# Optimization experiments

Measured on AMD Instinct MI355X. Metric: run time of the kernel, lower is better.

## Reference

```python
import jax, jax.numpy as jnp
import numpy as np

# Constants mirroring HomeostasisConfig defaults + STDP module constants
TARGET_RATE = 0.05
TRACE_DECAY = float(np.exp(-1.0 / 20.0))   # tau_plus = tau_minus = 20
ACT_DECAY   = 0.999                        # activity_decay / firing-rate EMA
BETA        = 0.9                          # LIF membrane leak
ETA_TH      = 0.001                        # threshold_adaptation_rate
MIN_W, MAX_W = -5.0, 5.0
MIN_TH, MAX_TH = 0.5, 2.0
LR          = 1.0                          # STDP learning_rate
TAG_THRESH  = 1e-3

B, T, IN, OUT = 128, 64, 2048, 2048


def setup_inputs() -> dict:
    key = jax.random.key(0)
    k1, k2 = jax.random.split(key, 2)
    # Bernoulli(0.1) rate-coded input spike trains (batch, time, in_features)
    x = (jax.random.uniform(k1, (B, T, IN)) < 0.1).astype(jnp.float32)
    W = jax.random.normal(k2, (OUT, IN), dtype=jnp.float32) * 0.1
    thresholds = jnp.ones((OUT,), dtype=jnp.float32)
    A_plus = jnp.asarray(0.01, dtype=jnp.float32)
    A_minus = jnp.asarray(0.012, dtype=jnp.float32)
    return {"x": x, "W": W, "thresholds": thresholds,
            "A_plus": A_plus, "A_minus": A_minus}


def _step(carry, x_t, A_plus, A_minus):
    v, Wc, th, pre_tr, post_tr, post_act, fr_ema, tags = carry
    # LIF membrane: leak + synaptic current, threshold, reset
    v = BETA * v + x_t @ Wc.T                      # (B, OUT)
    spk = (v >= th).astype(v.dtype)                # (B, OUT)
    v = v * (1.0 - spk)
    # trace / activity updates (batch-mean rates, as in update_traces)
    pre_rate = x_t.mean(axis=0)                    # (IN,)
    post_rate = spk.mean(axis=0)                   # (OUT,)
    pre_tr = TRACE_DECAY * pre_tr + pre_rate
    post_tr = TRACE_DECAY * post_tr + post_rate
    post_act = ACT_DECAY * post_act + (1.0 - ACT_DECAY) * post_rate
    # STDP: LTP/LTD outer products
    ltp = jnp.outer(post_rate, pre_tr) * jnp.abs(A_plus)
    ltd = jnp.outer(post_tr, pre_rate) * jnp.abs(A_minus)
    dw = ltp - ltd                                 # (OUT, IN)
    # metaplasticity factor
    meta = 1.0 / jnp.clip(post_act / TARGET_RATE, 0.5, 2.0)
    dw = dw * meta[:, None]
    # soft bounds
    w_range = MAX_W - MIN_W
    dw_b = jnp.where(dw > 0, dw * (MAX_W - Wc) / w_range,
                     dw * (Wc - MIN_W) / w_range)
    # synaptic tags
    tags = jnp.maximum(0.99 * tags, (jnp.abs(dw_b) > TAG_THRESH).astype(v.dtype))
    # apply STDP + clamp
    Wc = jnp.clip(Wc + LR * dw_b, MIN_W, MAX_W)
    # intrinsic plasticity: threshold homeostasis
    fr_ema = ACT_DECAY * fr_ema + (1.0 - ACT_DECAY) * post_rate
    th = jnp.clip(th * (1.0 + ETA_TH * (post_rate - TARGET_RATE)), MIN_TH, MAX_TH)
    return (v, Wc, th, pre_tr, post_tr, post_act, fr_ema, tags), spk


def reference(x, W, thresholds, A_plus, A_minus):
    b, t, n_in = x.shape
    n_out = W.shape[0]
    dt = x.dtype
    carry0 = (
        jnp.zeros((b, n_out), dt),                 # membrane potential
        W,                                         # weights
        thresholds,                                # per-neuron thresholds
        jnp.zeros((n_in,), dt),                    # pre trace
        jnp.zeros((n_out,), dt),                   # post trace
        jnp.full((n_out,), TARGET_RATE, dt),       # post activity EMA
        jnp.full((n_out,), TARGET_RATE, dt),       # firing-rate EMA
        jnp.zeros((n_out, n_in), dt),              # synaptic tags
    )
    step = lambda c, xt: _step(c, xt, A_plus, A_minus)
    _, spikes = jax.lax.scan(step, carry0, jnp.swapaxes(x, 0, 1))
    return jnp.swapaxes(spikes, 0, 1)              # (B, T, OUT)
```

## Files before the change

### kernel.cpp

```cpp
#include <hip/hip_runtime.h>
#include <cmath>

#define B_   128
#define T_   64
#define IN_  2048
#define OUT_ 2048
#define IDXSTRIDE 512

#define BETA_D   0.9
#define ACTDEC_D 0.999
#define ETA_TH_D 0.001
#define TARGET_D 0.05
#define MINW_D   (-5.0)
#define MAXW_D   (5.0)
#define MINTH_D  0.5
#define MAXTH_D  2.0

#define SWADR(i) (((unsigned)(i) << 6) | ((((unsigned)(i) ^ ((unsigned)(i) >> 2)) & 3u) << 4))
#define VL_OFF   131072
#define TH_OFF   139264
#define PTR_OFF  139328
#define PACT_OFF 139392
#define COA_OFF  139456
#define COB_OFF  139520
#define PART_OFF 139584
#define SMEM_BYTES 139840

__global__ __launch_bounds__(256) void k_rate(const float* __restrict__ x,
                                              double* __restrict__ pre_rate) {
    int t = blockIdx.x;
    int i = blockIdx.y * 256 + threadIdx.x;
    const float* xp = x + (size_t)t * IN_ + i;
    float s = 0.f;
    for (int b = 0; b < B_; ++b) s += xp[(size_t)b * T_ * IN_];
    pre_rate[(size_t)t * IN_ + i] = (double)s * (1.0 / 128.0);
}

__global__ __launch_bounds__(256) void k_scan(const double* __restrict__ pre_rate,
                                              double* __restrict__ pre_tr, double decay) {
    int i = blockIdx.x * 256 + threadIdx.x;
    double tr = 0.0;
    for (int t = 0; t < T_; ++t) {
        tr = decay * tr + pre_rate[(size_t)t * IN_ + i];
        pre_tr[(size_t)t * IN_ + i] = tr;
    }
}

__global__ __launch_bounds__(256) void k_build_idx(const float* __restrict__ x,
        unsigned* __restrict__ idx, int* __restrict__ cnt) {
    int row  = blockIdx.x * 4 + (threadIdx.x >> 6);
    int lane = threadIdx.x & 63;
    const float* xr = x + (size_t)row * IN_;
    unsigned* ip = idx + (size_t)row * IDXSTRIDE;
    int c = 0;
    for (int ch = 0; ch < IN_ / 64; ++ch) {
        int i = ch * 64 + lane;
        float vv = xr[i];
        unsigned long long m = __ballot(vv != 0.0f);
        if (vv != 0.0f) {
            int pos = c + __popcll(m & ((1ull << lane) - 1ull));
            if (pos < IDXSTRIDE) ip[pos] = SWADR(i);
        }
        c += __popcll(m);
    }
    if (lane == 0) cnt[row] = (c < IDXSTRIDE) ? c : IDXSTRIDE;
}

#define GAT(r, A0, A1) do { \
    const double2 w_ = *(const double2*)(smem + ((r) ^ cx)); \
    A0 += w_.x; A1 += w_.y; } while (0)

__global__ __launch_bounds__(512, 1) void k_main(
        const float* __restrict__ W, const float* __restrict__ thr,
        const float* __restrict__ Ap, const float* __restrict__ Am,
        const unsigned* __restrict__ idx, const int* __restrict__ cnt,
        const double* __restrict__ pre_rate, const double* __restrict__ pre_tr,
        float* __restrict__ out, double decay) {
    extern __shared__ char smem[];
    double* vL    = (double*)(smem + VL_OFF);
    double* thL   = (double*)(smem + TH_OFF);
    double* ptrL  = (double*)(smem + PTR_OFF);
    double* pactL = (double*)(smem + PACT_OFF);
    double* coaL  = (double*)(smem + COA_OFF);
    double* cobL  = (double*)(smem + COB_OFF);
    float*  part  = (float*)(smem + PART_OFF);

    const int tid = threadIdx.x;
    const int s   = blockIdx.x;

#pragma unroll
    for (int o = 0; o < 8; ++o) {
        const float* wr = W + (size_t)(s * 8 + o) * IN_;
        for (int i = tid; i < IN_; i += 512) {
            *(double*)(smem + ((SWADR(i) ^ ((unsigned)(o >> 1) << 4)) | ((unsigned)(o & 1) << 3)))
                = (double)wr[i];
        }
    }
    for (int e = tid; e < B_ * 8; e += 512) vL[e] = 0.0;
    if (tid < 8) {
        thL[tid]   = (double)thr[s * 8 + tid];
        ptrL[tid]  = 0.0;
        pactL[tid] = TARGET_D;
    }
    const double apv = fabs((double)Ap[0]);
    const double amv = fabs((double)Am[0]);
    __syncthreads();

    const int b  = tid >> 2;
    const int c2 = tid & 3;
    const unsigned cx = (unsigned)c2 << 4;

    for (int t = 0; t < T_; ++t) {
        int row = b * T_ + t;
        int n = cnt[row];
        const unsigned* ip = idx + (size_t)row * IDXSTRIDE;
        double a0 = 0.0, a1 = 0.0, b0 = 0.0, b1 = 0.0;
        int n8 = n & ~7;
        int j = 0;
        if (n8 > 0) {
            uint4 q0 = *(const uint4*)(ip);
            uint4 q1 = *(const uint4*)(ip + 4);
            for (;;) {
                uint4 qa = q0, qb = q1;
                int jn = j + 8;
                if (jn < n8) {
                    q0 = *(const uint4*)(ip + jn);
                    q1 = *(const uint4*)(ip + jn + 4);
                }
                GAT(qa.x, a0, a1); GAT(qa.y, b0, b1);
                GAT(qa.z, a0, a1); GAT(qa.w, b0, b1);
                GAT(qb.x, a0, a1); GAT(qb.y, b0, b1);
                GAT(qb.z, a0, a1); GAT(qb.w, b0, b1);
                j = jn;
                if (j >= n8) break;
            }
        }
        for (; j < n; ++j) { unsigned r = ip[j]; GAT(r, a0, a1); }
        a0 += b0; a1 += b1;

        double2 vv = *(double2*)&vL[b * 8 + c2 * 2];
        double v0 = BETA_D * vv.x + a0;
        double v1 = BETA_D * vv.y + a1;
        double t0 = thL[c2 * 2], t1 = thL[c2 * 2 + 1];
        float s0 = (v0 >= t0) ? 1.0f : 0.0f;
        float s1 = (v1 >= t1) ? 1.0f : 0.0f;
        *(float2*)(out + (size_t)row * OUT_ + s * 8 + c2 * 2) = make_float2(s0, s1);
        vv.x = (s0 != 0.0f) ? 0.0 : v0;
        vv.y = (s1 != 0.0f) ? 0.0 : v1;
        *(double2*)&vL[b * 8 + c2 * 2] = vv;

        float r0 = s0, r1 = s1;
        r0 += __shfl_xor(r0, 4);  r1 += __shfl_xor(r1, 4);
        r0 += __shfl_xor(r0, 8);  r1 += __shfl_xor(r1, 8);
        r0 += __shfl_xor(r0, 16); r1 += __shfl_xor(r1, 16);
        r0 += __shfl_xor(r0, 32); r1 += __shfl_xor(r1, 32);
        if ((tid & 63) < 4)
            *(float2*)&part[(tid >> 6) * 8 + c2 * 2] = make_float2(r0, r1);
        __syncthreads();

        if (tid < 8) {
            int c = tid;
            float cf = 0.f;
#pragma unroll
            for (int w8 = 0; w8 < 8; ++w8) cf += part[w8 * 8 + c];
            double prate = (double)cf * (1.0 / 128.0);
            double ptr2 = decay * ptrL[c] + prate;            ptrL[c] = ptr2;
            double pact = ACTDEC_D * pactL[c] + (1.0 - ACTDEC_D) * prate;  pactL[c] = pact;
            double r = pact / TARGET_D;
            r = r < 0.5 ? 0.5 : (r > 2.0 ? 2.0 : r);
            double meta = 1.0 / r;
            coaL[c] = apv * prate * meta;
            cobL[c] = amv * ptr2 * meta;
            double thv = thL[c] * (1.0 + ETA_TH_D * (prate - TARGET_D));
            thL[c] = thv < MINTH_D ? MINTH_D : (thv > MAXTH_D ? MAXTH_D : thv);
        }
        __syncthreads();

        if (t + 1 < T_) {
            double ca0 = coaL[c2 * 2], ca1 = coaL[c2 * 2 + 1];
            double cb0 = cobL[c2 * 2], cb1 = cobL[c2 * 2 + 1];
            const double* prt = pre_tr   + (size_t)t * IN_;
            const double* prr = pre_rate + (size_t)t * IN_;
#pragma unroll 4
            for (int k = 0; k < 16; ++k) {
                int i = k * 128 + b;
                double p = prt[i], q = prr[i];
                double2* wp = (double2*)(smem + (SWADR(i) ^ cx));
                double2 w2 = *wp;
                double dw0 = ca0 * p - cb0 * q;
                double dw1 = ca1 * p - cb1 * q;
                double dwb0 = dw0 > 0.0 ? (dw0 * (MAXW_D - w2.x)) / 10.0
                                        : (dw0 * (w2.x - MINW_D)) / 10.0;
                double dwb1 = dw1 > 0.0 ? (dw1 * (MAXW_D - w2.y)) / 10.0
                                        : (dw1 * (w2.y - MINW_D)) / 10.0;
                double nw0 = w2.x + dwb0;
                nw0 = nw0 < MINW_D ? MINW_D : (nw0 > MAXW_D ? MAXW_D : nw0);
                double nw1 = w2.y + dwb1;
                nw1 = nw1 < MINW_D ? MINW_D : (nw1 > MAXW_D ? MAXW_D : nw1);
                *wp = make_double2(nw0, nw1);
            }
        }
        __syncthreads();
    }
}

extern "C" void kernel_launch(void* const* d_in, const int* in_sizes, int n_in,
                              void* d_out, int out_size, void* d_ws, size_t ws_size,
                              hipStream_t stream) {
    const float* x   = (const float*)d_in[0];
    const float* W   = (const float*)d_in[1];
    const float* thr = (const float*)d_in[2];
    const float* Ap  = (const float*)d_in[3];
    const float* Am  = (const float*)d_in[4];
    float* out = (float*)d_out;
    char* ws = (char*)d_ws;

    double* pre_rate = (double*)(ws);
    double* pre_tr   = (double*)(ws + 1048576);
    unsigned* idx    = (unsigned*)(ws + 2097152);
    int* cnt         = (int*)(ws + 2097152 + 16777216);

    double decay = std::exp(-1.0 / 20.0);

    (void)hipFuncSetAttribute((const void*)k_main,
                              hipFuncAttributeMaxDynamicSharedMemorySize, SMEM_BYTES);

    k_rate<<<dim3(T_, IN_ / 256), 256, 0, stream>>>(x, pre_rate);
    k_scan<<<IN_ / 256, 256, 0, stream>>>(pre_rate, pre_tr, decay);
    k_build_idx<<<(B_ * T_) / 4, 256, 0, stream>>>(x, idx, cnt);
    k_main<<<256, 512, SMEM_BYTES, stream>>>(W, thr, Ap, Am, idx, cnt,
                                             pre_rate, pre_tr, out, decay);
}
```

Before: 879.3 us.

## Split gather across two threads per output pair and drop serial stats phase

Block size goes from 512 to 1024 threads. The index list is split into even and odd halves, so two threads gather each batch/output pair and combine their sums with a shuffle. The per-neuron statistics (traces, activity, thresholds) are now held redundantly in registers by every thread instead of being computed by 8 threads between two barriers, which removes one __syncthreads per step. Spike counts go through double-buffered shared atomics. The shared-memory swizzle is dropped, which may raise bank conflicts; more waves may help hide LDS gather latency.

```diff
diff --git a/kernel.cpp b/kernel.cpp
--- a/kernel.cpp
+++ b/kernel.cpp
@@ -6,6 +6,7 @@
 #define IN_  2048
 #define OUT_ 2048
 #define IDXSTRIDE 512
+#define HALFSTRIDE 256
 
 #define BETA_D   0.9
 #define ACTDEC_D 0.999
@@ -16,15 +17,8 @@
 #define MINTH_D  0.5
 #define MAXTH_D  2.0
 
-#define SWADR(i) (((unsigned)(i) << 6) | ((((unsigned)(i) ^ ((unsigned)(i) >> 2)) & 3u) << 4))
-#define VL_OFF   131072
-#define TH_OFF   139264
-#define PTR_OFF  139328
-#define PACT_OFF 139392
-#define COA_OFF  139456
-#define COB_OFF  139520
-#define PART_OFF 139584
-#define SMEM_BYTES 139840
+#define PART_OFF   131072
+#define SMEM_BYTES 131136
 
 __global__ __launch_bounds__(256) void k_rate(const float* __restrict__ x,
                                               double* __restrict__ pre_rate) {
@@ -52,69 +46,80 @@
     int lane = threadIdx.x & 63;
     const float* xr = x + (size_t)row * IN_;
     unsigned* ip = idx + (size_t)row * IDXSTRIDE;
-    int c = 0;
+    const unsigned long long EVEN = 0x5555555555555555ull;
+    unsigned long long below = (1ull << lane) - 1ull;
+    int ce = 0, co = 0;
     for (int ch = 0; ch < IN_ / 64; ++ch) {
         int i = ch * 64 + lane;
         float vv = xr[i];
         unsigned long long m = __ballot(vv != 0.0f);
+        unsigned long long me = m & EVEN, mo = m & ~EVEN;
         if (vv != 0.0f) {
-            int pos = c + __popcll(m & ((1ull << lane) - 1ull));
-            if (pos < IDXSTRIDE) ip[pos] = SWADR(i);
-        }
-        c += __popcll(m);
-    }
-    if (lane == 0) cnt[row] = (c < IDXSTRIDE) ? c : IDXSTRIDE;
+            if ((lane & 1) == 0) {
+                int pos = ce + __popcll(me & below);
+                if (pos < HALFSTRIDE) ip[pos] = (unsigned)i << 6;
+            } else {
+                int pos = co + __popcll(mo & below);
+                if (pos < HALFSTRIDE) ip[HALFSTRIDE + pos] = (unsigned)i << 6;
+            }
+        }
+        ce += __popcll(me);
+        co += __popcll(mo);
+    }
+    if (lane == 0) {
+        if (ce > HALFSTRIDE) ce = HALFSTRIDE;
+        if (co > HALFSTRIDE) co = HALFSTRIDE;
+        cnt[row] = ce | (co << 16);
+    }
 }
 
 #define GAT(r, A0, A1) do { \
     const double2 w_ = *(const double2*)(smem + ((r) ^ cx)); \
     A0 += w_.x; A1 += w_.y; } while (0)
 
-__global__ __launch_bounds__(512, 1) void k_main(
+__global__ __launch_bounds__(1024, 4) void k_main(
         const float* __restrict__ W, const float* __restrict__ thr,
         const float* __restrict__ Ap, const float* __restrict__ Am,
         const unsigned* __restrict__ idx, const int* __restrict__ cnt,
         const double* __restrict__ pre_rate, const double* __restrict__ pre_tr,
         float* __restrict__ out, double decay) {
     extern __shared__ char smem[];
-    double* vL    = (double*)(smem + VL_OFF);
-    double* thL   = (double*)(smem + TH_OFF);
-    double* ptrL  = (double*)(smem + PTR_OFF);
-    double* pactL = (double*)(smem + PACT_OFF);
-    double* coaL  = (double*)(smem + COA_OFF);
-    double* cobL  = (double*)(smem + COB_OFF);
-    float*  part  = (float*)(smem + PART_OFF);
-
-    const int tid = threadIdx.x;
-    const int s   = blockIdx.x;
+    float* part = (float*)(smem + PART_OFF);
+
+    const int tid  = threadIdx.x;
+    const int s    = blockIdx.x;
+    const int lane = tid & 63;
+    const int h    = tid & 1;
+    const int c2   = (tid >> 1) & 3;
+    const int b    = tid >> 3;
+    const unsigned cx = (unsigned)c2 << 4;
 
 #pragma unroll
     for (int o = 0; o < 8; ++o) {
         const float* wr = W + (size_t)(s * 8 + o) * IN_;
-        for (int i = tid; i < IN_; i += 512) {
-            *(double*)(smem + ((SWADR(i) ^ ((unsigned)(o >> 1) << 4)) | ((unsigned)(o & 1) << 3)))
-                = (double)wr[i];
-        }
-    }
-    for (int e = tid; e < B_ * 8; e += 512) vL[e] = 0.0;
-    if (tid < 8) {
-        thL[tid]   = (double)thr[s * 8 + tid];
-        ptrL[tid]  = 0.0;
-        pactL[tid] = TARGET_D;
-    }
+        for (int i = tid; i < IN_; i += 1024) {
+            *(double*)(smem + (((unsigned)i << 6) | ((unsigned)(o >> 1) << 4)
+                               | ((unsigned)(o & 1) << 3))) = (double)wr[i];
+        }
+    }
+    if (tid < 16) part[tid] = 0.0f;
+
+    double th0 = (double)thr[s * 8 + c2 * 2];
+    double th1 = (double)thr[s * 8 + c2 * 2 + 1];
+    double ptr0 = 0.0, ptr1 = 0.0;
+    double pact0 = TARGET_D, pact1 = TARGET_D;
+    double vr0 = 0.0, vr1 = 0.0;
     const double apv = fabs((double)Ap[0]);
     const double amv = fabs((double)Am[0]);
     __syncthreads();
 
-    const int b  = tid >> 2;
-    const int c2 = tid & 3;
-    const unsigned cx = (unsigned)c2 << 4;
-
     for (int t = 0; t < T_; ++t) {
+        const int pb = t & 1;
         int row = b * T_ + t;
-        int n = cnt[row];
-        const unsigned* ip = idx + (size_t)row * IDXSTRIDE;
-        double a0 = 0.0, a1 = 0.0, b0 = 0.0, b1 = 0.0;
+        int cc = cnt[row];
+        int n = h ? (cc >> 16) : (cc & 0xffff);
+        const unsigned* ip = idx + (size_t)row * IDXSTRIDE + h * HALFSTRIDE;
+        double a0 = 0.0, a1 = 0.0, e0 = 0.0, e1 = 0.0;
         int n8 = n & ~7;
         int j = 0;
         if (n8 > 0) {
@@ -127,65 +132,73 @@
                     q0 = *(const uint4*)(ip + jn);
                     q1 = *(const uint4*)(ip + jn + 4);
                 }
-                GAT(qa.x, a0, a1); GAT(qa.y, b0, b1);
-                GAT(qa.z, a0, a1); GAT(qa.w, b0, b1);
-                GAT(qb.x, a0, a1); GAT(qb.y, b0, b1);
-                GAT(qb.z, a0, a1); GAT(qb.w, b0, b1);
+                GAT(qa.x, a0, a1); GAT(qa.y, e0, e1);
+                GAT(qa.z, a0, a1); GAT(qa.w, e0, e1);
+                GAT(qb.x, a0, a1); GAT(qb.y, e0, e1);
+                GAT(qb.z, a0, a1); GAT(qb.w, e0, e1);
                 j = jn;
                 if (j >= n8) break;
             }
         }
         for (; j < n; ++j) { unsigned r = ip[j]; GAT(r, a0, a1); }
-        a0 += b0; a1 += b1;
-
-        double2 vv = *(double2*)&vL[b * 8 + c2 * 2];
-        double v0 = BETA_D * vv.x + a0;
-        double v1 = BETA_D * vv.y + a1;
-        double t0 = thL[c2 * 2], t1 = thL[c2 * 2 + 1];
-        float s0 = (v0 >= t0) ? 1.0f : 0.0f;
-        float s1 = (v1 >= t1) ? 1.0f : 0.0f;
-        *(float2*)(out + (size_t)row * OUT_ + s * 8 + c2 * 2) = make_float2(s0, s1);
-        vv.x = (s0 != 0.0f) ? 0.0 : v0;
-        vv.y = (s1 != 0.0f) ? 0.0 : v1;
-        *(double2*)&vL[b * 8 + c2 * 2] = vv;
-
-        float r0 = s0, r1 = s1;
-        r0 += __shfl_xor(r0, 4);  r1 += __shfl_xor(r1, 4);
-        r0 += __shfl_xor(r0, 8);  r1 += __shfl_xor(r1, 8);
-        r0 += __shfl_xor(r0, 16); r1 += __shfl_xor(r1, 16);
-        r0 += __shfl_xor(r0, 32); r1 += __shfl_xor(r1, 32);
-        if ((tid & 63) < 4)
-            *(float2*)&part[(tid >> 6) * 8 + c2 * 2] = make_float2(r0, r1);
-        __syncthreads();
-
-        if (tid < 8) {
-            int c = tid;
-            float cf = 0.f;
-#pragma unroll
-            for (int w8 = 0; w8 < 8; ++w8) cf += part[w8 * 8 + c];
-            double prate = (double)cf * (1.0 / 128.0);
-            double ptr2 = decay * ptrL[c] + prate;            ptrL[c] = ptr2;
-            double pact = ACTDEC_D * pactL[c] + (1.0 - ACTDEC_D) * prate;  pactL[c] = pact;
-            double r = pact / TARGET_D;
-            r = r < 0.5 ? 0.5 : (r > 2.0 ? 2.0 : r);
-            double meta = 1.0 / r;
-            coaL[c] = apv * prate * meta;
-            cobL[c] = amv * ptr2 * meta;
-            double thv = thL[c] * (1.0 + ETA_TH_D * (prate - TARGET_D));
-            thL[c] = thv < MINTH_D ? MINTH_D : (thv > MAXTH_D ? MAXTH_D : thv);
-        }
-        __syncthreads();
+        a0 += e0; a1 += e1;
+        a0 += __shfl_xor(a0, 1);
+        a1 += __shfl_xor(a1, 1);
+
+        float s0 = 0.f, s1 = 0.f;
+        if (h == 0) {
+            double v0 = BETA_D * vr0 + a0;
+            double v1 = BETA_D * vr1 + a1;
+            s0 = (v0 >= th0) ? 1.0f : 0.0f;
+            s1 = (v1 >= th1) ? 1.0f : 0.0f;
+            *(float2*)(out + (size_t)row * OUT_ + s * 8 + c2 * 2) = make_float2(s0, s1);
+            vr0 = (s0 != 0.0f) ? 0.0 : v0;
+            vr1 = (s1 != 0.0f) ? 0.0 : v1;
+        }
 
         if (t + 1 < T_) {
-            double ca0 = coaL[c2 * 2], ca1 = coaL[c2 * 2 + 1];
-            double cb0 = cobL[c2 * 2], cb1 = cobL[c2 * 2 + 1];
+            float r0 = s0, r1 = s1;
+            r0 += __shfl_xor(r0, 8);  r1 += __shfl_xor(r1, 8);
+            r0 += __shfl_xor(r0, 16); r1 += __shfl_xor(r1, 16);
+            r0 += __shfl_xor(r0, 32); r1 += __shfl_xor(r1, 32);
+            if (lane < 8 && (lane & 1) == 0) {
+                atomicAdd(&part[pb * 8 + c2 * 2], r0);
+                atomicAdd(&part[pb * 8 + c2 * 2 + 1], r1);
+            }
+            if (tid < 8) part[(pb ^ 1) * 8 + tid] = 0.0f;
+            __syncthreads();
+
+            float cf0 = part[pb * 8 + c2 * 2];
+            float cf1 = part[pb * 8 + c2 * 2 + 1];
+            double prate0 = (double)cf0 * (1.0 / 128.0);
+            double prate1 = (double)cf1 * (1.0 / 128.0);
+            ptr0 = decay * ptr0 + prate0;
+            ptr1 = decay * ptr1 + prate1;
+            pact0 = ACTDEC_D * pact0 + (1.0 - ACTDEC_D) * prate0;
+            pact1 = ACTDEC_D * pact1 + (1.0 - ACTDEC_D) * prate1;
+            double r_ = pact0 / TARGET_D;
+            r_ = r_ < 0.5 ? 0.5 : (r_ > 2.0 ? 2.0 : r_);
+            double meta0 = 1.0 / r_;
+            r_ = pact1 / TARGET_D;
+            r_ = r_ < 0.5 ? 0.5 : (r_ > 2.0 ? 2.0 : r_);
+            double meta1 = 1.0 / r_;
+            double ca0 = apv * prate0 * meta0;
+            double ca1 = apv * prate1 * meta1;
+            double cb0 = amv * ptr0 * meta0;
+            double cb1 = amv * ptr1 * meta1;
+            double thv = th0 * (1.0 + ETA_TH_D * (prate0 - TARGET_D));
+            th0 = thv < MINTH_D ? MINTH_D : (thv > MAXTH_D ? MAXTH_D : thv);
+            thv = th1 * (1.0 + ETA_TH_D * (prate1 - TARGET_D));
+            th1 = thv < MINTH_D ? MINTH_D : (thv > MAXTH_D ? MAXTH_D : thv);
+
             const double* prt = pre_tr   + (size_t)t * IN_;
             const double* prr = pre_rate + (size_t)t * IN_;
-#pragma unroll 4
-            for (int k = 0; k < 16; ++k) {
-                int i = k * 128 + b;
+            const int b2 = (b << 1) | h;
+#pragma unroll
+            for (int k = 0; k < 8; ++k) {
+                int i = k * 256 + b2;
                 double p = prt[i], q = prr[i];
-                double2* wp = (double2*)(smem + (SWADR(i) ^ cx));
+                double2* wp = (double2*)(smem + (((unsigned)i << 6) | cx));
                 double2 w2 = *wp;
                 double dw0 = ca0 * p - cb0 * q;
                 double dw1 = ca1 * p - cb1 * q;
@@ -199,8 +212,8 @@
                 nw1 = nw1 < MINW_D ? MINW_D : (nw1 > MAXW_D ? MAXW_D : nw1);
                 *wp = make_double2(nw0, nw1);
             }
-        }
-        __syncthreads();
+            __syncthreads();
+        }
     }
 }
 
@@ -228,6 +241,6 @@
     k_rate<<<dim3(T_, IN_ / 256), 256, 0, stream>>>(x, pre_rate);
     k_scan<<<IN_ / 256, 256, 0, stream>>>(pre_rate, pre_tr, decay);
     k_build_idx<<<(B_ * T_) / 4, 256, 0, stream>>>(x, idx, cnt);
-    k_main<<<256, 512, SMEM_BYTES, stream>>>(W, thr, Ap, Am, idx, cnt,
-                                             pre_rate, pre_tr, out, decay);
-}
+    k_main<<<256, 1024, SMEM_BYTES, stream>>>(W, thr, Ap, Am, idx, cnt,
+                                              pre_rate, pre_tr, out, decay);
+}
```

Result: faster. 835.3 us (-5.0%).
